# Performance work log

Hardware: AMD Instinct MI355X
Metric: run time of the kernel (lower is better)

Reference implementation:

```python
import jax, jax.numpy as jnp
import numpy as np

B, S, H, DH = 8, 2048, 16, 64
D = H * DH  # 1024; also the input feature dim
BIG_NEG = 1e8


def setup_inputs() -> dict:
    key = jax.random.key(0)
    ks = jax.random.split(key, 7)
    glorot = lambda k, shp: jax.random.normal(k, shp, jnp.float32) * np.sqrt(2.0 / (shp[0] + shp[1]))
    return {
        "Q_seq": jax.random.normal(ks[0], (B, S, D), jnp.float32),
        "K_seq": jax.random.normal(ks[1], (B, S, D), jnp.float32),
        "Q_mask": jnp.ones((B, S), jnp.float32),
        "K_mask": jnp.ones((B, S), jnp.float32),
        "WQ": glorot(ks[2], (D, D)),
        "WK": glorot(ks[3], (D, D)),
        "Wq": glorot(ks[4], (D, H)),
        "Wk": glorot(ks[5], (D, H)),
        "WP": glorot(ks[6], (D, D)),
    }


def reference(Q_seq, B_K_seq=None, **_unused):
    raise NotImplementedError  # placeholder overwritten below


def reference(Q_seq, K_seq, Q_mask, K_mask, WQ, WK, Wq, Wk, WP):
    scale = 1.0 / (DH ** 0.5)
    b, s, _ = Q_seq.shape

    Q = Q_seq @ WQ                                        # (B,S,D)
    # query additive attention over the sequence, per head
    q_logits = jnp.einsum('bsd,dh->bhs', Q, Wq) * scale   # (B,H,S)
    q_logits = q_logits - (1.0 - Q_mask[:, None, :]) * BIG_NEG
    q_att = jax.nn.softmax(q_logits, axis=-1)

    Qh = Q.reshape(b, s, H, DH).transpose(0, 2, 1, 3)     # (B,H,S,DH)
    Kh = (K_seq @ WK).reshape(b, s, H, DH).transpose(0, 2, 1, 3)

    global_q = jnp.einsum('bhs,bhsd->bhd', q_att, Qh)     # (B,H,DH)
    QK = Kh * global_q[:, :, None, :]                     # (B,H,S,DH)

    # NOTE: original reshapes (B,H,S,DH) straight to (B,S,H*DH) WITHOUT a
    # transpose (head-mixing raw reshape) — replicated faithfully here.
    QK_flat = QK.reshape(b, s, H * DH)
    k_logits = jnp.einsum('bsd,dh->bhs', QK_flat, Wk) * scale
    k_logits = k_logits - (1.0 - K_mask[:, None, :]) * BIG_NEG
    k_att = jax.nn.softmax(k_logits, axis=-1)

    global_k = jnp.einsum('bhs,bhsd->bhd', k_att, QK)     # (B,H,DH)
    QKQ = global_k[:, :, None, :] * Qh                    # (B,H,S,DH)

    out = QKQ.transpose(0, 2, 1, 3).reshape(b, s, H * DH) @ WP
    out = out.reshape(b, s, H, DH).transpose(0, 2, 1, 3) + Qh   # (B,H,S,DH)
    out = out.transpose(0, 2, 1, 3).reshape(b, s, H * DH)       # (B,S,D)
    return out
```

## Files before the change

### kernel.cpp

```cpp
#include <hip/hip_runtime.h>
#include <cstdint>
#include <cstddef>


#define B_ 8
#define S_ 2048
#define H_ 16
#define D_ 1024
#define SCALE_ 0.125f
#define BIGNEG_ 1e8f

typedef __attribute__((ext_vector_type(8))) __bf16 bf16x8;
typedef __attribute__((ext_vector_type(4))) float f32x4;

__device__ __forceinline__ unsigned short f2bf(float f) {
  unsigned int u = __float_as_uint(f);
  u += 0x7FFFu + ((u >> 16) & 1u);
  return (unsigned short)(u >> 16);
}
__device__ __forceinline__ float bf2f(unsigned short h) {
  return __uint_as_float(((unsigned int)h) << 16);
}

__device__ __forceinline__ void gll16(const void* g, void* l) {
  __builtin_amdgcn_global_load_lds(
      (__attribute__((address_space(1))) void*)(uintptr_t)g,
      (__attribute__((address_space(3))) void*)(uintptr_t)l,
      16, 0, 0);
}

__global__ __launch_bounds__(256) void k_conv2(
    const float* __restrict__ in0, unsigned short* __restrict__ out0,
    const float* __restrict__ in1, unsigned short* __restrict__ out1, int n4) {
  int i = blockIdx.x * 256 + threadIdx.x;
  const float* in = in0;
  unsigned short* out = out0;
  if (i >= n4) { i -= n4; in = in1; out = out1; }
  float4 v = ((const float4*)in)[i];
  ushort4 o;
  o.x = f2bf(v.x); o.y = f2bf(v.y); o.z = f2bf(v.z); o.w = f2bf(v.w);
  ((ushort4*)out)[i] = o;
}

__global__ __launch_bounds__(256) void k_transpose3(
    const float* __restrict__ s0, unsigned short* __restrict__ d0,
    const float* __restrict__ s1, unsigned short* __restrict__ d1,
    const float* __restrict__ s2, unsigned short* __restrict__ d2,
    int K, int N) {
  const float* src = blockIdx.z == 0 ? s0 : (blockIdx.z == 1 ? s1 : s2);
  unsigned short* dst = blockIdx.z == 0 ? d0 : (blockIdx.z == 1 ? d1 : d2);
  __shared__ float tile[32][33];
  int n0 = blockIdx.x * 32, k0 = blockIdx.y * 32;
  int tx = threadIdx.x, ty = threadIdx.y;
#pragma unroll
  for (int i = 0; i < 4; i++) {
    int r = ty + i * 8;
    if (k0 + r < K && n0 + tx < N) tile[r][tx] = src[(size_t)(k0 + r) * N + n0 + tx];
  }
  __syncthreads();
#pragma unroll
  for (int i = 0; i < 4; i++) {
    int rn = ty + i * 8;
    if (n0 + rn < N && k0 + tx < K)
      dst[(size_t)(n0 + rn) * K + k0 + tx] = f2bf(tile[tx][rn]);
  }
}

__global__ __launch_bounds__(256) void k_transpose2(
    const float* __restrict__ s0, unsigned short* __restrict__ d0,
    const float* __restrict__ s1, unsigned short* __restrict__ d1,
    int K, int N) {
  const float* src = blockIdx.z == 0 ? s0 : s1;
  unsigned short* dst = blockIdx.z == 0 ? d0 : d1;
  __shared__ float tile[32][33];
  int n0 = blockIdx.x * 32, k0 = blockIdx.y * 32;
  int tx = threadIdx.x, ty = threadIdx.y;
#pragma unroll
  for (int i = 0; i < 4; i++) {
    int r = ty + i * 8;
    if (k0 + r < K && n0 + tx < N) tile[r][tx] = src[(size_t)(k0 + r) * N + n0 + tx];
  }
  __syncthreads();
#pragma unroll
  for (int i = 0; i < 4; i++) {
    int rn = ty + i * 8;
    if (n0 + rn < N && k0 + tx < K)
      dst[(size_t)(n0 + rn) * K + k0 + tx] = f2bf(tile[tx][rn]);
  }
}

__global__ __launch_bounds__(512, 1) void k_gemm256(
    const unsigned short* __restrict__ A, const unsigned short* __restrict__ Aalt,
    int asplit,
    const unsigned short* __restrict__ BTa, const unsigned short* __restrict__ BTb,
    int bstride, int bshift,
    unsigned short* __restrict__ Cbf, unsigned short* __restrict__ Calt,
    float* __restrict__ Cf, const unsigned short* __restrict__ Res,
    int N, int K, int ntiles) {
  __shared__ unsigned short lds[65536];
  int t = threadIdx.x;
  int lid = (blockIdx.x & 7) * ((int)gridDim.x >> 3) + (blockIdx.x >> 3);
  int mt = lid / ntiles, nt = lid - mt * ntiles;
  const unsigned short* BT = BTa;
  unsigned short* Cb = Cbf;
  if (mt >= asplit) { mt -= asplit; A = Aalt; BT = BTb; Cb = Calt; }
  if (bstride) BT += (size_t)(mt >> bshift) * (size_t)bstride;
  int m0 = mt * 256, n0 = nt * 256;
  int lane = t & 63, w = t >> 6;
  int wr = (w >> 2) * 128;
  int wc = (w & 3) * 64;
  int mq = lane & 15, q = lane >> 4;

  f32x4 zero = {0.f, 0.f, 0.f, 0.f};
  f32x4 acc[8][4];
#pragma unroll
  for (int i = 0; i < 8; i++)
#pragma unroll
    for (int j = 0; j < 4; j++) acc[i][j] = zero;

  const unsigned short* gA[2];
  const unsigned short* gB[2];
  int oA[2], oB[2];
#pragma unroll
  for (int p = 0; p < 2; p++) {
    int g = t + p * 512;
    int row2 = g >> 3, pre = (g & 7) ^ (row2 & 7);
    int r = row2 * 2 + (pre >> 2), oct = pre & 3;
    gA[p] = A + (size_t)(m0 + r) * K + oct * 8;
    gB[p] = BT + (size_t)(n0 + r) * K + oct * 8;
    oA[p] = g * 8;
    oB[p] = 8192 + g * 8;
  }

  int sA8 = ((((mq & 1) << 2) | q) ^ (mq >> 1)) * 8;
  int ra = (wr >> 1) + (mq >> 1);
  int rb = (wc >> 1) + (mq >> 1);

  int NT = K >> 5;
#pragma unroll
  for (int Tt = 0; Tt < 3; Tt++) {
    int ks = Tt * 32, sb = Tt << 14;
#pragma unroll
    for (int p = 0; p < 2; p++) gll16(gA[p] + ks, &lds[sb + oA[p]]);
#pragma unroll
    for (int p = 0; p < 2; p++) gll16(gB[p] + ks, &lds[sb + oB[p]]);
  }
  asm volatile("s_waitcnt vmcnt(8)" ::: "memory");
  __builtin_amdgcn_s_barrier();
  __builtin_amdgcn_sched_barrier(0);

  for (int T = 0; T < NT; ++T) {
    const int base = (T & 3) << 14;
    const unsigned short* la = &lds[base];
    const unsigned short* lb = &lds[base + 8192];
    const int sbase = ((T + 3) & 3) << 14;
    const int ks = (T + 3) * 32;
    const bool stg = (T + 3 < NT);

    bf16x8 avA[4], bv[4];
#pragma unroll
    for (int i = 0; i < 4; i++)
      avA[i] = *(const bf16x8*)&la[(ra + i * 8) * 64 + sA8];
#pragma unroll
    for (int j = 0; j < 4; j++)
      bv[j] = *(const bf16x8*)&lb[(rb + j * 8) * 64 + sA8];
    if (stg) {
      gll16(gA[0] + ks, &lds[sbase + oA[0]]);
      gll16(gB[0] + ks, &lds[sbase + oB[0]]);
    }
    __builtin_amdgcn_s_barrier();
    asm volatile("s_waitcnt lgkmcnt(0)" ::: "memory");
    __builtin_amdgcn_sched_barrier(0);
    __builtin_amdgcn_s_setprio(1);
#pragma unroll
    for (int i = 0; i < 4; i++)
#pragma unroll
      for (int j = 0; j < 4; j++)
        acc[i][j] = __builtin_amdgcn_mfma_f32_16x16x32_bf16(avA[i], bv[j], acc[i][j], 0, 0, 0);
    __builtin_amdgcn_s_setprio(0);
    __builtin_amdgcn_sched_barrier(0);

    bf16x8 avB[4];
#pragma unroll
    for (int i = 0; i < 4; i++)
      avB[i] = *(const bf16x8*)&la[(ra + (i + 4) * 8) * 64 + sA8];
    if (stg) {
      gll16(gA[1] + ks, &lds[sbase + oA[1]]);
      gll16(gB[1] + ks, &lds[sbase + oB[1]]);
    }
    __builtin_amdgcn_s_barrier();
    asm volatile("s_waitcnt lgkmcnt(0)" ::: "memory");
    __builtin_amdgcn_sched_barrier(0);
    __builtin_amdgcn_s_setprio(1);
#pragma unroll
    for (int i = 0; i < 4; i++)
#pragma unroll
      for (int j = 0; j < 4; j++)
        acc[i + 4][j] = __builtin_amdgcn_mfma_f32_16x16x32_bf16(avB[i], bv[j], acc[i + 4][j], 0, 0, 0);
    __builtin_amdgcn_s_setprio(0);
    __builtin_amdgcn_sched_barrier(0);

    if (T <= NT - 4) {
      asm volatile("s_waitcnt vmcnt(8)" ::: "memory");
    } else if (T == NT - 3) {
      asm volatile("s_waitcnt vmcnt(4)" ::: "memory");
    } else {
      asm volatile("s_waitcnt vmcnt(0)" ::: "memory");
    }
    __builtin_amdgcn_s_barrier();
    __builtin_amdgcn_sched_barrier(0);
  }

#pragma unroll
  for (int i = 0; i < 8; i++)
#pragma unroll
    for (int j = 0; j < 4; j++)
#pragma unroll
      for (int r = 0; r < 4; r++) {
        int row = m0 + wr + i * 16 + q * 4 + r;
        int col = n0 + wc + j * 16 + mq;
        size_t o = (size_t)row * N + col;
        float v = acc[i][j][r];
        if (Res) v += bf2f(Res[o]);
        if (Cf) Cf[o] = v;
        if (Cb) Cb[o] = f2bf(v);
      }
}

__global__ __launch_bounds__(256) void k_logits16(
    const unsigned short* __restrict__ A,
    const unsigned short* __restrict__ BT16,
    const float* __restrict__ mask,
    float* __restrict__ outl,
    int K) {
  __shared__ unsigned short lA[64 * 32];
  int t = threadIdx.x;
  int m0 = blockIdx.x * 64;
  int lane = t & 63, w = t >> 6;
  int mq = lane & 15, q = lane >> 4;
  f32x4 acc = {0.f, 0.f, 0.f, 0.f};
  const unsigned short* gA = A + (size_t)(m0 + (t >> 2)) * K + (t & 3) * 8;
  unsigned short* pA = &lA[t * 8];
  for (int k0 = 0; k0 < K; k0 += 32) {
    gll16(gA + k0, pA);
    bf16x8 bv = *(const bf16x8*)&BT16[(size_t)mq * K + k0 + q * 8];
    __syncthreads();
    bf16x8 a0 = *(const bf16x8*)&lA[(w * 16 + mq) * 32 + q * 8];
    acc = __builtin_amdgcn_mfma_f32_16x16x32_bf16(a0, bv, acc, 0, 0, 0);
    __syncthreads();
  }
#pragma unroll
  for (int r = 0; r < 4; r++) {
    int row = m0 + w * 16 + q * 4 + r;
    int b = row >> 11, s = row & 2047;
    float v = acc[r] * SCALE_ - (1.0f - mask[row]) * BIGNEG_;
    outl[((size_t)(b * 16 + mq)) * 2048 + s] = v;
  }
}

__global__ __launch_bounds__(256) void k_logits16g(
    const unsigned short* __restrict__ Khbf,
    const unsigned short* __restrict__ WkT,
    const float* __restrict__ gq,
    const float* __restrict__ mask,
    float* __restrict__ outl) {
  __shared__ unsigned short lA[64 * 32];
  int t = threadIdx.x;
  int m0 = blockIdx.x * 64;
  int bb = m0 >> 11;
  int h2 = (m0 >> 7) & 15;
  int half = (m0 >> 6) & 1;
  int lane = t & 63, w = t >> 6;
  int mq = lane & 15, q = lane >> 4;
  f32x4 acc = {0.f, 0.f, 0.f, 0.f};
  int r0 = half * 64 + (t >> 2);
  int c0 = t & 3;
  const unsigned short* base = Khbf + (size_t)bb * 2048 * 1024 + h2 * 64;
  const float* gqb = gq + bb * 1024 + h2 * 64;
  unsigned short* pA = &lA[t * 8];
  for (int k0 = 0; k0 < 1024; k0 += 32) {
    int kc0 = k0 + c0 * 8;
    gll16(base + (size_t)(16 * r0 + (kc0 >> 6)) * 1024 + (kc0 & 63), pA);
    int kq = k0 + q * 8;
    bf16x8 wv = *(const bf16x8*)&WkT[(size_t)mq * 1024 + kq];
    float4 g0 = *(const float4*)&gqb[kq & 63];
    float4 g1 = *(const float4*)&gqb[(kq & 63) + 4];
    bf16x8 bv;
    bv[0] = (__bf16)((float)wv[0] * g0.x);
    bv[1] = (__bf16)((float)wv[1] * g0.y);
    bv[2] = (__bf16)((float)wv[2] * g0.z);
    bv[3] = (__bf16)((float)wv[3] * g0.w);
    bv[4] = (__bf16)((float)wv[4] * g1.x);
    bv[5] = (__bf16)((float)wv[5] * g1.y);
    bv[6] = (__bf16)((float)wv[6] * g1.z);
    bv[7] = (__bf16)((float)wv[7] * g1.w);
    __syncthreads();
    bf16x8 a0 = *(const bf16x8*)&lA[(w * 16 + mq) * 32 + q * 8];
    acc = __builtin_amdgcn_mfma_f32_16x16x32_bf16(a0, bv, acc, 0, 0, 0);
    __syncthreads();
  }
#pragma unroll
  for (int r = 0; r < 4; r++) {
    int row = m0 + w * 16 + q * 4 + r;
    int b = row >> 11, s = row & 2047;
    float v = acc[r] * SCALE_ - (1.0f - mask[row]) * BIGNEG_;
    outl[((size_t)(b * 16 + mq)) * 2048 + s] = v;
  }
}

__global__ __launch_bounds__(256) void k_softmax(float* __restrict__ logits) {
  __shared__ float red[8];
  int t = threadIdx.x;
  int lane = t & 63, w = t >> 6;
  float* lg = logits + (size_t)blockIdx.x * 2048;
  float4 a = ((const float4*)lg)[t];
  float4 b = ((const float4*)lg)[t + 256];
  float mx = fmaxf(fmaxf(fmaxf(a.x, a.y), fmaxf(a.z, a.w)),
                   fmaxf(fmaxf(b.x, b.y), fmaxf(b.z, b.w)));
#pragma unroll
  for (int off = 32; off > 0; off >>= 1) mx = fmaxf(mx, __shfl_down(mx, off, 64));
  if (lane == 0) red[w] = mx;
  __syncthreads();
  mx = fmaxf(fmaxf(red[0], red[1]), fmaxf(red[2], red[3]));
  float4 ea, eb;
  ea.x = expf(a.x - mx); ea.y = expf(a.y - mx); ea.z = expf(a.z - mx); ea.w = expf(a.w - mx);
  eb.x = expf(b.x - mx); eb.y = expf(b.y - mx); eb.z = expf(b.z - mx); eb.w = expf(b.w - mx);
  float ps = ea.x + ea.y + ea.z + ea.w + eb.x + eb.y + eb.z + eb.w;
#pragma unroll
  for (int off = 32; off > 0; off >>= 1) ps += __shfl_down(ps, off, 64);
  if (lane == 0) red[4 + w] = ps;
  __syncthreads();
  float inv = 1.0f / (red[4] + red[5] + red[6] + red[7]);
  ea.x *= inv; ea.y *= inv; ea.z *= inv; ea.w *= inv;
  eb.x *= inv; eb.y *= inv; eb.z *= inv; eb.w *= inv;
  ((float4*)lg)[t] = ea;
  ((float4*)lg)[t + 256] = eb;
}

__global__ __launch_bounds__(256) void k_poolpart(
    const float* __restrict__ att,
    const unsigned short* __restrict__ X,
    float* __restrict__ partial) {
  __shared__ float satt[32 * 16];
  int c = blockIdx.x, b = blockIdx.y;
  int t = threadIdx.x;
  for (int i = t; i < 512; i += 256) {
    int sl = i >> 4, h = i & 15;
    satt[i] = att[(((size_t)b * 16 + h) << 11) + c * 32 + sl];
  }
  __syncthreads();
  int h = t >> 4;
  const ushort4* xp = (const ushort4*)X + ((size_t)b * 2048 + c * 32) * 256 + t;
  float4 acc = {0.f, 0.f, 0.f, 0.f};
#pragma unroll 8
  for (int sl = 0; sl < 32; sl++) {
    float av = satt[sl * 16 + h];
    ushort4 xv = xp[sl * 256];
    acc.x += av * bf2f(xv.x);
    acc.y += av * bf2f(xv.y);
    acc.z += av * bf2f(xv.z);
    acc.w += av * bf2f(xv.w);
  }
  ((float4*)partial)[((size_t)b * 64 + c) * 256 + t] = acc;
}

__global__ __launch_bounds__(256) void k_poolfin(
    const float* __restrict__ partial,
    const float* __restrict__ gmul,
    float* __restrict__ outp) {
  int oi = blockIdx.x * 256 + threadIdx.x;
  int b = oi >> 10;
  const float* pp = partial + (size_t)b * 64 * 1024 + (oi & 1023);
  float s = 0.f;
#pragma unroll 8
  for (int c = 0; c < 64; c++) s += pp[(size_t)c * 1024];
  if (gmul) s *= gmul[oi];
  outp[oi] = s;
}

__global__ __launch_bounds__(256) void k_wpb(
    const unsigned short* __restrict__ WPT,
    const float* __restrict__ gk,
    unsigned short* __restrict__ WPb) {
  int i = blockIdx.x * 256 + threadIdx.x;
  int flat4 = i * 4;
  int b = flat4 >> 20;
  int rem = flat4 & 1048575;
  int k = rem & 1023;
  ushort4 wv = *(const ushort4*)&WPT[rem];
  float4 gv = *(const float4*)&gk[b * 1024 + k];
  ushort4 o;
  o.x = f2bf(bf2f(wv.x) * gv.x);
  o.y = f2bf(bf2f(wv.y) * gv.y);
  o.z = f2bf(bf2f(wv.z) * gv.z);
  o.w = f2bf(bf2f(wv.w) * gv.w);
  *(ushort4*)&WPb[flat4] = o;
}

extern "C" void kernel_launch(void* const* d_in, const int* in_sizes, int n_in,
                              void* d_out, int out_size, void* d_ws, size_t ws_size,
                              hipStream_t stream) {
  const float* Qseq  = (const float*)d_in[0];
  const float* Kseq  = (const float*)d_in[1];
  const float* Qmask = (const float*)d_in[2];
  const float* Kmask = (const float*)d_in[3];
  const float* WQ    = (const float*)d_in[4];
  const float* WK    = (const float*)d_in[5];
  const float* Wq    = (const float*)d_in[6];
  const float* Wk    = (const float*)d_in[7];
  const float* WP    = (const float*)d_in[8];
  float* out = (float*)d_out;

  const size_t SD = (size_t)B_ * S_ * D_;
  unsigned short* Qbf  = (unsigned short*)d_ws;
  unsigned short* Khbf = Qbf + SD;
  unsigned short* buf0 = Khbf + SD;
  unsigned short* WQT  = buf0 + SD;
  unsigned short* WKT  = WQT + (size_t)D_ * D_;
  unsigned short* WPT  = WKT + (size_t)D_ * D_;
  unsigned short* WqT  = WPT + (size_t)D_ * D_;
  unsigned short* WkT  = WqT + (size_t)H_ * D_;
  float* ql = (float*)(WkT + (size_t)H_ * D_);
  float* kl = ql + (size_t)B_ * H_ * S_;
  float* gq = kl + (size_t)B_ * H_ * S_;
  float* gk = gq + (size_t)B_ * D_;
  float* partial = (float*)buf0;
  unsigned short* WPb = buf0 + 2 * 1024 * 1024;
  unsigned short* Kstage = (unsigned short*)d_out;

  dim3 blk256(256);
  dim3 blk512(512);
  dim3 tblk(32, 8);
  int n4 = (int)(SD / 4);

  k_transpose3<<<dim3(32, 32, 3), tblk, 0, stream>>>(WQ, WQT, WK, WKT, WP, WPT, D_, D_);
  k_transpose2<<<dim3(1, 32, 2), tblk, 0, stream>>>(Wq, WqT, Wk, WkT, D_, H_);

  k_conv2<<<dim3(2 * ((n4 + 255) / 256)), blk256, 0, stream>>>(Qseq, buf0, Kseq, Kstage, n4);

  k_gemm256<<<dim3(512), blk512, 0, stream>>>(buf0, Kstage, 64, WQT, WKT, 0, 0,
                                              Qbf, Khbf, (float*)nullptr,
                                              (const unsigned short*)nullptr, D_, D_, 4);

  k_logits16<<<dim3(256), blk256, 0, stream>>>(Qbf, WqT, Qmask, ql, D_);
  k_softmax<<<dim3(128), blk256, 0, stream>>>(ql);
  k_poolpart<<<dim3(64, 8), blk256, 0, stream>>>(ql, Qbf, partial);
  k_poolfin<<<dim3(32), blk256, 0, stream>>>(partial, (const float*)nullptr, gq);

  k_logits16g<<<dim3(256), blk256, 0, stream>>>(Khbf, WkT, gq, Kmask, kl);
  k_softmax<<<dim3(128), blk256, 0, stream>>>(kl);
  k_poolpart<<<dim3(64, 8), blk256, 0, stream>>>(kl, Khbf, partial);
  k_poolfin<<<dim3(32), blk256, 0, stream>>>(partial, gq, gk);

  k_wpb<<<dim3(8192), blk256, 0, stream>>>(WPT, gk, WPb);
  k_gemm256<<<dim3(256), blk512, 0, stream>>>(Qbf, Qbf, 1 << 30, WPb, WPb, 1 << 20, 3,
                                              (unsigned short*)nullptr, (unsigned short*)nullptr,
                                              out, Qbf, D_, D_, 4);
}
```

Before: 388.2 us.

## Split GEMM main loop into four interleaved MFMA/LDS/prefetch phases

Restructures each K-step of the bf16 MFMA GEMM main loop from two phases into four. The LDS fragment reads and the global-to-LDS prefetches are spread one per phase between smaller 8-MFMA clusters, with the B fragments loaded in two halves. The goal is to overlap memory traffic with MFMA work at a finer grain and lower peak register pressure. It adds an extra barrier per phase, which could cost more than the overlap gains.

Result: no change. 391.3 us (+0.8%).

```diff
diff --git a/kernel.cpp b/kernel.cpp
--- a/kernel.cpp
+++ b/kernel.cpp
@@ -156,18 +156,15 @@
     const int sbase = ((T + 3) & 3) << 14;
     const int ks = (T + 3) * 32;
     const bool stg = (T + 3 < NT);
-
-    bf16x8 avA[4], bv[4];
+    bf16x8 avA[4], avB[4], bv[4];
+
 #pragma unroll
     for (int i = 0; i < 4; i++)
       avA[i] = *(const bf16x8*)&la[(ra + i * 8) * 64 + sA8];
 #pragma unroll
-    for (int j = 0; j < 4; j++)
+    for (int j = 0; j < 2; j++)
       bv[j] = *(const bf16x8*)&lb[(rb + j * 8) * 64 + sA8];
-    if (stg) {
-      gll16(gA[0] + ks, &lds[sbase + oA[0]]);
-      gll16(gB[0] + ks, &lds[sbase + oB[0]]);
-    }
+    if (stg) gll16(gA[0] + ks, &lds[sbase + oA[0]]);
     __builtin_amdgcn_s_barrier();
     asm volatile("s_waitcnt lgkmcnt(0)" ::: "memory");
     __builtin_amdgcn_sched_barrier(0);
@@ -175,19 +172,15 @@
 #pragma unroll
     for (int i = 0; i < 4; i++)
 #pragma unroll
-      for (int j = 0; j < 4; j++)
+      for (int j = 0; j < 2; j++)
         acc[i][j] = __builtin_amdgcn_mfma_f32_16x16x32_bf16(avA[i], bv[j], acc[i][j], 0, 0, 0);
     __builtin_amdgcn_s_setprio(0);
     __builtin_amdgcn_sched_barrier(0);
 
-    bf16x8 avB[4];
-#pragma unroll
-    for (int i = 0; i < 4; i++)
-      avB[i] = *(const bf16x8*)&la[(ra + (i + 4) * 8) * 64 + sA8];
-    if (stg) {
-      gll16(gA[1] + ks, &lds[sbase + oA[1]]);
-      gll16(gB[1] + ks, &lds[sbase + oB[1]]);
-    }
+#pragma unroll
+    for (int j = 2; j < 4; j++)
+      bv[j] = *(const bf16x8*)&lb[(rb + j * 8) * 64 + sA8];
+    if (stg) gll16(gB[0] + ks, &lds[sbase + oB[0]]);
     __builtin_amdgcn_s_barrier();
     asm volatile("s_waitcnt lgkmcnt(0)" ::: "memory");
     __builtin_amdgcn_sched_barrier(0);
@@ -195,11 +188,36 @@
 #pragma unroll
     for (int i = 0; i < 4; i++)
 #pragma unroll
-      for (int j = 0; j < 4; j++)
+      for (int j = 2; j < 4; j++)
+        acc[i][j] = __builtin_amdgcn_mfma_f32_16x16x32_bf16(avA[i], bv[j], acc[i][j], 0, 0, 0);
+    __builtin_amdgcn_s_setprio(0);
+    __builtin_amdgcn_sched_barrier(0);
+
+#pragma unroll
+    for (int i = 0; i < 4; i++)
+      avB[i] = *(const bf16x8*)&la[(ra + (i + 4) * 8) * 64 + sA8];
+    if (stg) gll16(gA[1] + ks, &lds[sbase + oA[1]]);
+    __builtin_amdgcn_s_barrier();
+    asm volatile("s_waitcnt lgkmcnt(0)" ::: "memory");
+    __builtin_amdgcn_sched_barrier(0);
+    __builtin_amdgcn_s_setprio(1);
+#pragma unroll
+    for (int i = 0; i < 4; i++)
+#pragma unroll
+      for (int j = 2; j < 4; j++)
         acc[i + 4][j] = __builtin_amdgcn_mfma_f32_16x16x32_bf16(avB[i], bv[j], acc[i + 4][j], 0, 0, 0);
     __builtin_amdgcn_s_setprio(0);
     __builtin_amdgcn_sched_barrier(0);
 
+    if (stg) gll16(gB[1] + ks, &lds[sbase + oB[1]]);
+    __builtin_amdgcn_s_setprio(1);
+#pragma unroll
+    for (int i = 0; i < 4; i++)
+#pragma unroll
+      for (int j = 0; j < 2; j++)
+        acc[i + 4][j] = __builtin_amdgcn_mfma_f32_16x16x32_bf16(avB[i], bv[j], acc[i + 4][j], 0, 0, 0);
+    __builtin_amdgcn_s_setprio(0);
+    __builtin_amdgcn_sched_barrier(0);
     if (T <= NT - 4) {
       asm volatile("s_waitcnt vmcnt(8)" ::: "memory");
     } else if (T == NT - 3) {
```
